# Kernel optimization log

Hardware: AMD Instinct MI355X
Metric: run time of the kernel (lower is better)

The kernel has to match this reference:

```python
import jax, jax.numpy as jnp
import numpy as np
from jax import lax

WINDOW_SIZE = 11
SIGMA = 1.5
MAX_VAL = 1.0


def _gaussian_kernel_2d(window_size: int, sigma: float) -> jnp.ndarray:
    coords = jnp.arange(window_size, dtype=jnp.float32) - window_size // 2
    g = jnp.exp(-coords ** 2 / (2.0 * sigma ** 2))
    g = g / g.sum()
    k2d = jnp.outer(g, g)
    return k2d / k2d.sum()  # [W, W]


def _depthwise_conv(x: jnp.ndarray, k2d: jnp.ndarray) -> jnp.ndarray:
    # x: [B, C, H, W]; depthwise (groups=C) conv with SAME padding
    C = x.shape[1]
    ws = k2d.shape[0]
    kernel = jnp.broadcast_to(k2d[None, None], (C, 1, ws, ws)).astype(x.dtype)  # [C,1,ws,ws]
    pad = ws // 2
    return lax.conv_general_dilated(
        x, kernel,
        window_strides=(1, 1),
        padding=((pad, pad), (pad, pad)),
        dimension_numbers=('NCHW', 'OIHW', 'NCHW'),
        feature_group_count=C,
    )


def setup_inputs() -> dict:
    key = jax.random.key(0)
    k1, k2 = jax.random.split(key)
    B, C, H, W = 16, 3, 512, 512
    sr = jax.random.uniform(k1, (B, C, H, W), dtype=jnp.float32)
    hr = jax.random.uniform(k2, (B, C, H, W), dtype=jnp.float32)
    return {"sr": sr, "hr": hr}


def reference(sr, hr):
    c1 = (0.01 * MAX_VAL) ** 2
    c2 = (0.03 * MAX_VAL) ** 2
    k2d = _gaussian_kernel_2d(WINDOW_SIZE, SIGMA)

    mu1 = _depthwise_conv(sr, k2d)
    mu2 = _depthwise_conv(hr, k2d)
    mu1_sq = mu1 ** 2
    mu2_sq = mu2 ** 2
    mu1_mu2 = mu1 * mu2
    sigma1_sq = _depthwise_conv(sr * sr, k2d) - mu1_sq
    sigma2_sq = _depthwise_conv(hr * hr, k2d) - mu2_sq
    sigma12 = _depthwise_conv(sr * hr, k2d) - mu1_mu2

    ssim_map = (2 * mu1_mu2 + c1) * (2 * sigma12 + c2) / (
        (mu1_sq + mu2_sq + c1) * (sigma1_sq + sigma2_sq + c2) + 1e-12)
    return 1.0 - ssim_map.mean()
```

## Files before the change

### kernel.cpp

```cpp
#include <hip/hip_runtime.h>


typedef __attribute__((ext_vector_type(2))) float  f32x2;
typedef __attribute__((ext_vector_type(4))) float  f32x4;
typedef __fp16 f16;
typedef __attribute__((ext_vector_type(2))) __fp16 h2v;
typedef __attribute__((ext_vector_type(4))) __fp16 h4;
typedef __attribute__((ext_vector_type(8))) __fp16 h8;

constexpr int IMG_H = 512;
constexpr int IMG_W = 512;
constexpr int PL    = IMG_H * IMG_W;
constexpr int NBC   = 48;
constexpr int TW    = 64;
constexpr int TH    = 32;
constexpr int NBLKX = IMG_W / TW;
constexpr int NBLKY = IMG_H / TH;
constexpr int NPERS = 1024;
constexpr int ITERS = NBLKX * NBLKY * NBC / NPERS;

constexpr int XP   = 104;
constexpr int XR   = 48;
constexpr int XQS  = XR * XP;
constexpr int HTP  = 72;
constexpr int HTQS = 64 * HTP;
constexpr int SMEMH = 4 * XQS;
static_assert(4 * HTQS <= SMEMH, "Ht must fit in X union");

constexpr float C1 = 1.0e-4f;
constexpr float C2 = 9.0e-4f;

__device__ const float GW[11] = {
    0.00102838f, 0.00759876f, 0.03600077f, 0.10936070f, 0.21300553f,
    0.26601172f, 0.21300553f, 0.10936070f, 0.03600077f, 0.00759876f,
    0.00102838f};

__device__ __forceinline__ h8 ldfrag(const f16* __restrict__ gtab, int base) {
    h8 b;
#pragma unroll
    for (int i = 0; i < 8; ++i) b[i] = gtab[base + i];
    return b;
}

__global__ __launch_bounds__(64) void ssim_init(double* acc) {
    if (threadIdx.x == 0) acc[0] = 0.0;
}

__global__ __launch_bounds__(256, 4) void ssim_main(const float* __restrict__ sr,
                                                    const float* __restrict__ hr,
                                                    double* __restrict__ sink,
                                                    int mode) {
    __shared__ __align__(16) f16 smem[SMEMH];
    __shared__ __align__(8)  f16 gtab[128];
    __shared__ float wsums[4];

    const int tid  = threadIdx.x;
    const int w    = tid >> 6;
    const int lane = tid & 63;
    const int l15  = lane & 15;
    const int grp8 = (lane >> 4) << 3;
    const int grp4 = (lane >> 4) << 2;

    const int bx  = blockIdx.x & 7;
    const int by  = (blockIdx.x >> 3) & 15;
    const int bc0 = blockIdx.x >> 7;
    const int gr0 = by * TH - 5;
    const int gc0 = bx * TW - 8;

    const float* __restrict__ srp = sr + (size_t)bc0 * PL;
    const float* __restrict__ hrp = hr + (size_t)bc0 * PL;
    const size_t PSTEP = (size_t)8 * PL;

    const int c8  = tid & 15;
    const int r0s = tid >> 4;
    unsigned okm = 0;
    int off[3];
#pragma unroll
    for (int t = 0; t < 3; ++t) {
        const int r  = r0s + 16 * t;
        const int gr = gr0 + r;
        const int gc = gc0 + c8 * 8;
        if ((c8 < 10) & (r < 42) &
            ((unsigned)gr < (unsigned)IMG_H) & ((unsigned)gc < (unsigned)IMG_W))
            okm |= (1u << t);
        off[t] = gr * IMG_W + gc;
    }

    if (tid < 128) {
        const int d = tid - 66;
        float v = 0.f;
        if ((unsigned)d <= 10u) v = GW[d];
        gtab[tid] = (f16)v;
    }

    float s16 = 0.f;
#pragma unroll
    for (int d = 0; d <= 10; ++d) s16 += (float)(f16)GW[d];
    const float rs = 1.0f / (s16 * s16);

    float4 La0[3], La1[3], Lb0[3], Lb1[3];
#pragma unroll
    for (int t = 0; t < 3; ++t) {
        La0[t] = La1[t] = Lb0[t] = Lb1[t] = (float4){0.f, 0.f, 0.f, 0.f};
        if (okm & (1u << t)) {
            const float4* pa = (const float4*)&srp[off[t]];
            const float4* pb = (const float4*)&hrp[off[t]];
            La0[t] = pa[0]; La1[t] = pa[1];
            Lb0[t] = pb[0]; Lb1[t] = pb[1];
        }
    }
    __syncthreads();

    const h8 bh = ldfrag(gtab, 63 + grp8 - l15);
    const h8 bv = ldfrag(gtab, 66 + grp8 - l15);

    float local = 0.f;

    for (int iter = 0; iter < ITERS; ++iter) {
        if (c8 < 10) {
#pragma unroll
            for (int t = 0; t < 3; ++t) {
                const int r = r0s + 16 * t;
                const f32x2* a0 = (const f32x2*)&La0[t];
                const f32x2* a1 = (const f32x2*)&La1[t];
                const f32x2* b0 = (const f32x2*)&Lb0[t];
                const f32x2* b1 = (const f32x2*)&Lb1[t];
                const f32x2 s0 = a0[0] * a0[0] + b0[0] * b0[0];
                const f32x2 s1 = a0[1] * a0[1] + b0[1] * b0[1];
                const f32x2 s2 = a1[0] * a1[0] + b1[0] * b1[0];
                const f32x2 s3 = a1[1] * a1[1] + b1[1] * b1[1];
                const f32x2 p0 = a0[0] * b0[0], p1 = a0[1] * b0[1];
                const f32x2 p2 = a1[0] * b1[0], p3 = a1[1] * b1[1];
                union { h2v h2[4]; h8 v; } uva, uvb, uss, uab;
                uva.h2[0] = __builtin_amdgcn_cvt_pkrtz(a0[0].x, a0[0].y);
                uva.h2[1] = __builtin_amdgcn_cvt_pkrtz(a0[1].x, a0[1].y);
                uva.h2[2] = __builtin_amdgcn_cvt_pkrtz(a1[0].x, a1[0].y);
                uva.h2[3] = __builtin_amdgcn_cvt_pkrtz(a1[1].x, a1[1].y);
                uvb.h2[0] = __builtin_amdgcn_cvt_pkrtz(b0[0].x, b0[0].y);
                uvb.h2[1] = __builtin_amdgcn_cvt_pkrtz(b0[1].x, b0[1].y);
                uvb.h2[2] = __builtin_amdgcn_cvt_pkrtz(b1[0].x, b1[0].y);
                uvb.h2[3] = __builtin_amdgcn_cvt_pkrtz(b1[1].x, b1[1].y);
                uss.h2[0] = __builtin_amdgcn_cvt_pkrtz(s0.x, s0.y);
                uss.h2[1] = __builtin_amdgcn_cvt_pkrtz(s1.x, s1.y);
                uss.h2[2] = __builtin_amdgcn_cvt_pkrtz(s2.x, s2.y);
                uss.h2[3] = __builtin_amdgcn_cvt_pkrtz(s3.x, s3.y);
                uab.h2[0] = __builtin_amdgcn_cvt_pkrtz(p0.x, p0.y);
                uab.h2[1] = __builtin_amdgcn_cvt_pkrtz(p1.x, p1.y);
                uab.h2[2] = __builtin_amdgcn_cvt_pkrtz(p2.x, p2.y);
                uab.h2[3] = __builtin_amdgcn_cvt_pkrtz(p3.x, p3.y);
                const int o = r * XP + c8 * 8;
                *(h8*)&smem[0 * XQS + o] = uva.v;
                *(h8*)&smem[1 * XQS + o] = uvb.v;
                *(h8*)&smem[2 * XQS + o] = uss.v;
                *(h8*)&smem[3 * XQS + o] = uab.v;
            }
        }
        __syncthreads();

        if (iter < ITERS - 1) {
            srp += PSTEP; hrp += PSTEP;
#pragma unroll
            for (int t = 0; t < 3; ++t) {
                if (okm & (1u << t)) {
                    const float4* pa = (const float4*)&srp[off[t]];
                    const float4* pb = (const float4*)&hrp[off[t]];
                    La0[t] = pa[0]; La1[t] = pa[1];
                    Lb0[t] = pb[0]; Lb1[t] = pb[1];
                }
            }
        }

        f32x4 acc[4][3] = {};
#pragma unroll
        for (int Mt = 0; Mt < 3; ++Mt) {
            const int arow = (16 * Mt + l15) * XP + 16 * w + grp8;
#pragma unroll
            for (int q = 0; q < 4; ++q) {
                const h8 af = *(const h8*)&smem[q * XQS + arow];
                acc[q][Mt] = __builtin_amdgcn_mfma_f32_16x16x32_f16(af, bh, acc[q][Mt], 0, 0, 0);
            }
        }
        __syncthreads();

#pragma unroll
        for (int q = 0; q < 4; ++q) {
#pragma unroll
            for (int Mt = 0; Mt < 3; ++Mt) {
                union { h2v h2[2]; h4 v; } u;
                u.h2[0] = __builtin_amdgcn_cvt_pkrtz(acc[q][Mt][0], acc[q][Mt][1]);
                u.h2[1] = __builtin_amdgcn_cvt_pkrtz(acc[q][Mt][2], acc[q][Mt][3]);
                *(h4*)&smem[q * HTQS + (16 * w + l15) * HTP + 16 * Mt + grp4] = u.v;
            }
        }

        f32x4 acc2[4][2] = {};
        const int abase = (16 * w + l15) * HTP + grp8;
#pragma unroll
        for (int q = 0; q < 4; ++q) {
            const h8 a0 = *(const h8*)&smem[q * HTQS + abase];
            const h8 a1 = *(const h8*)&smem[q * HTQS + abase + 16];
            acc2[q][0] = __builtin_amdgcn_mfma_f32_16x16x32_f16(a0, bv, acc2[q][0], 0, 0, 0);
            acc2[q][1] = __builtin_amdgcn_mfma_f32_16x16x32_f16(a1, bv, acc2[q][1], 0, 0, 0);
        }

#pragma unroll
        for (int nt = 0; nt < 2; ++nt) {
            const f32x4 m1 = acc2[0][nt] * rs;
            const f32x4 m2 = acc2[1][nt] * rs;
            const f32x4 S  = acc2[2][nt] * rs;
            const f32x4 pp = acc2[3][nt] * rs;
            const f32x4 mu1s = m1 * m1, mu2s = m2 * m2, mu12 = m1 * m2;
            const f32x4 sg12 = pp - mu12;
            const f32x4 sgs  = S - mu1s - mu2s;
            const f32x4 num = (2.f * mu12 + C1) * (2.f * sg12 + C2);
            const f32x4 den = (mu1s + mu2s + C1) * (sgs + C2) + 1e-12f;
#pragma unroll
            for (int e = 0; e < 4; ++e)
                local += num[e] * __builtin_amdgcn_rcpf(den[e]);
        }
        __syncthreads();
    }

#pragma unroll
    for (int offr = 32; offr > 0; offr >>= 1)
        local += __shfl_down(local, offr, 64);
    if ((tid & 63) == 0) wsums[tid >> 6] = local;
    __syncthreads();
    if (tid == 0) {
        const double bsum = (double)(wsums[0] + wsums[1] + wsums[2] + wsums[3]);
        if (mode == 0) {
            sink[blockIdx.x] = bsum;
        } else {
            atomicAdd(sink, bsum);
        }
    }
}

__global__ __launch_bounds__(256) void ssim_finalize(const double* __restrict__ partial,
                                                     float* __restrict__ out, int count) {
    __shared__ double ws[4];
    double s = 0.0;
    for (int i = threadIdx.x; i < count; i += 256) s += partial[i];
#pragma unroll
    for (int off = 32; off > 0; off >>= 1)
        s += __shfl_down(s, off, 64);
    const int lane = threadIdx.x & 63, wave = threadIdx.x >> 6;
    if (lane == 0) ws[wave] = s;
    __syncthreads();
    if (threadIdx.x == 0) {
        const double tot = ws[0] + ws[1] + ws[2] + ws[3];
        const double n = (double)NBC * IMG_H * IMG_W;
        out[0] = (float)(1.0 - tot / n);
    }
}

extern "C" void kernel_launch(void* const* d_in, const int* in_sizes, int n_in,
                              void* d_out, int out_size, void* d_ws, size_t ws_size,
                              hipStream_t stream) {
    const float* sr = (const float*)d_in[0];
    const float* hr = (const float*)d_in[1];
    float* out = (float*)d_out;

    if (ws_size >= (size_t)NPERS * sizeof(double)) {
        double* partial = (double*)d_ws;
        ssim_main<<<dim3(NPERS), dim3(256), 0, stream>>>(sr, hr, partial, 0);
        ssim_finalize<<<dim3(1), dim3(256), 0, stream>>>(partial, out, NPERS);
    } else {
        double* acc = (double*)d_ws;
        ssim_init<<<dim3(1), dim3(64), 0, stream>>>(acc);
        ssim_main<<<dim3(NPERS), dim3(256), 0, stream>>>(sr, hr, acc, 1);
        ssim_finalize<<<dim3(1), dim3(256), 0, stream>>>(acc, out, 1);
    }
}
```

Before: 130.0 us.

## Load MFMA A-fragments directly from global, drop input LDS staging and barriers

Each lane now loads its horizontal-pass MFMA A fragment straight from global memory into registers, converts it to fp16 and feeds the MFMA. This removes the shared-memory staging of the four input planes and all block-level barriers, since each wave only touches its own LDS rows for the transposed intermediate. Shared memory shrinks, occupancy is raised to 5 blocks per CU, and the persistent grid becomes 1280 blocks striding over planes by 10. The cost is that overlapping halo columns are loaded redundantly by several waves, and the software prefetch of the next plane is lost.

```diff
diff --git a/kernel.cpp b/kernel.cpp
--- a/kernel.cpp
+++ b/kernel.cpp
@@ -14,18 +14,11 @@
 constexpr int NBC   = 48;
 constexpr int TW    = 64;
 constexpr int TH    = 32;
-constexpr int NBLKX = IMG_W / TW;
-constexpr int NBLKY = IMG_H / TH;
-constexpr int NPERS = 1024;
-constexpr int ITERS = NBLKX * NBLKY * NBC / NPERS;
-
-constexpr int XP   = 104;
-constexpr int XR   = 48;
-constexpr int XQS  = XR * XP;
-constexpr int HTP  = 72;
-constexpr int HTQS = 64 * HTP;
-constexpr int SMEMH = 4 * XQS;
-static_assert(4 * HTQS <= SMEMH, "Ht must fit in X union");
+constexpr int NPERS = 1280;
+
+constexpr int HTP   = 56;
+constexpr int HTQS  = 64 * HTP;
+constexpr int SMEMH = 4 * HTQS;
 
 constexpr float C1 = 1.0e-4f;
 constexpr float C2 = 9.0e-4f;
@@ -46,7 +39,7 @@
     if (threadIdx.x == 0) acc[0] = 0.0;
 }
 
-__global__ __launch_bounds__(256, 4) void ssim_main(const float* __restrict__ sr,
+__global__ __launch_bounds__(256, 5) void ssim_main(const float* __restrict__ sr,
                                                     const float* __restrict__ hr,
                                                     double* __restrict__ sink,
                                                     int mode) {
@@ -67,24 +60,9 @@
     const int gr0 = by * TH - 5;
     const int gc0 = bx * TW - 8;
 
-    const float* __restrict__ srp = sr + (size_t)bc0 * PL;
-    const float* __restrict__ hrp = hr + (size_t)bc0 * PL;
-    const size_t PSTEP = (size_t)8 * PL;
-
-    const int c8  = tid & 15;
-    const int r0s = tid >> 4;
-    unsigned okm = 0;
-    int off[3];
-#pragma unroll
-    for (int t = 0; t < 3; ++t) {
-        const int r  = r0s + 16 * t;
-        const int gr = gr0 + r;
-        const int gc = gc0 + c8 * 8;
-        if ((c8 < 10) & (r < 42) &
-            ((unsigned)gr < (unsigned)IMG_H) & ((unsigned)gc < (unsigned)IMG_W))
-            okm |= (1u << t);
-        off[t] = gr * IMG_W + gc;
-    }
+    const int colh = gc0 + 16 * w + grp8;
+    const bool cok = (unsigned)colh < (unsigned)IMG_W;
+    const int rb   = gr0 + l15;
 
     if (tid < 128) {
         const int d = tid - 66;
@@ -98,17 +76,6 @@
     for (int d = 0; d <= 10; ++d) s16 += (float)(f16)GW[d];
     const float rs = 1.0f / (s16 * s16);
 
-    float4 La0[3], La1[3], Lb0[3], Lb1[3];
-#pragma unroll
-    for (int t = 0; t < 3; ++t) {
-        La0[t] = La1[t] = Lb0[t] = Lb1[t] = (float4){0.f, 0.f, 0.f, 0.f};
-        if (okm & (1u << t)) {
-            const float4* pa = (const float4*)&srp[off[t]];
-            const float4* pb = (const float4*)&hrp[off[t]];
-            La0[t] = pa[0]; La1[t] = pa[1];
-            Lb0[t] = pb[0]; Lb1[t] = pb[1];
-        }
-    }
     __syncthreads();
 
     const h8 bh = ldfrag(gtab, 63 + grp8 - l15);
@@ -116,72 +83,58 @@
 
     float local = 0.f;
 
-    for (int iter = 0; iter < ITERS; ++iter) {
-        if (c8 < 10) {
-#pragma unroll
-            for (int t = 0; t < 3; ++t) {
-                const int r = r0s + 16 * t;
-                const f32x2* a0 = (const f32x2*)&La0[t];
-                const f32x2* a1 = (const f32x2*)&La1[t];
-                const f32x2* b0 = (const f32x2*)&Lb0[t];
-                const f32x2* b1 = (const f32x2*)&Lb1[t];
-                const f32x2 s0 = a0[0] * a0[0] + b0[0] * b0[0];
-                const f32x2 s1 = a0[1] * a0[1] + b0[1] * b0[1];
-                const f32x2 s2 = a1[0] * a1[0] + b1[0] * b1[0];
-                const f32x2 s3 = a1[1] * a1[1] + b1[1] * b1[1];
-                const f32x2 p0 = a0[0] * b0[0], p1 = a0[1] * b0[1];
-                const f32x2 p2 = a1[0] * b1[0], p3 = a1[1] * b1[1];
-                union { h2v h2[4]; h8 v; } uva, uvb, uss, uab;
-                uva.h2[0] = __builtin_amdgcn_cvt_pkrtz(a0[0].x, a0[0].y);
-                uva.h2[1] = __builtin_amdgcn_cvt_pkrtz(a0[1].x, a0[1].y);
-                uva.h2[2] = __builtin_amdgcn_cvt_pkrtz(a1[0].x, a1[0].y);
-                uva.h2[3] = __builtin_amdgcn_cvt_pkrtz(a1[1].x, a1[1].y);
-                uvb.h2[0] = __builtin_amdgcn_cvt_pkrtz(b0[0].x, b0[0].y);
-                uvb.h2[1] = __builtin_amdgcn_cvt_pkrtz(b0[1].x, b0[1].y);
-                uvb.h2[2] = __builtin_amdgcn_cvt_pkrtz(b1[0].x, b1[0].y);
-                uvb.h2[3] = __builtin_amdgcn_cvt_pkrtz(b1[1].x, b1[1].y);
-                uss.h2[0] = __builtin_amdgcn_cvt_pkrtz(s0.x, s0.y);
-                uss.h2[1] = __builtin_amdgcn_cvt_pkrtz(s1.x, s1.y);
-                uss.h2[2] = __builtin_amdgcn_cvt_pkrtz(s2.x, s2.y);
-                uss.h2[3] = __builtin_amdgcn_cvt_pkrtz(s3.x, s3.y);
-                uab.h2[0] = __builtin_amdgcn_cvt_pkrtz(p0.x, p0.y);
-                uab.h2[1] = __builtin_amdgcn_cvt_pkrtz(p1.x, p1.y);
-                uab.h2[2] = __builtin_amdgcn_cvt_pkrtz(p2.x, p2.y);
-                uab.h2[3] = __builtin_amdgcn_cvt_pkrtz(p3.x, p3.y);
-                const int o = r * XP + c8 * 8;
-                *(h8*)&smem[0 * XQS + o] = uva.v;
-                *(h8*)&smem[1 * XQS + o] = uvb.v;
-                *(h8*)&smem[2 * XQS + o] = uss.v;
-                *(h8*)&smem[3 * XQS + o] = uab.v;
+    for (int bc = bc0; bc < NBC; bc += 10) {
+        const float* __restrict__ srp = sr + (size_t)bc * PL;
+        const float* __restrict__ hrp = hr + (size_t)bc * PL;
+
+        f32x4 acc[4][3] = {};
+#pragma unroll
+        for (int Mt = 0; Mt < 3; ++Mt) {
+            const int r  = rb + 16 * Mt;
+            const bool ok = cok & ((unsigned)r < (unsigned)IMG_H);
+            float4 a0, a1, b0, b1;
+            a0 = a1 = b0 = b1 = (float4){0.f, 0.f, 0.f, 0.f};
+            if (ok) {
+                const float4* pa = (const float4*)&srp[r * IMG_W + colh];
+                const float4* pb = (const float4*)&hrp[r * IMG_W + colh];
+                a0 = pa[0]; a1 = pa[1];
+                b0 = pb[0]; b1 = pb[1];
             }
-        }
-        __syncthreads();
-
-        if (iter < ITERS - 1) {
-            srp += PSTEP; hrp += PSTEP;
-#pragma unroll
-            for (int t = 0; t < 3; ++t) {
-                if (okm & (1u << t)) {
-                    const float4* pa = (const float4*)&srp[off[t]];
-                    const float4* pb = (const float4*)&hrp[off[t]];
-                    La0[t] = pa[0]; La1[t] = pa[1];
-                    Lb0[t] = pb[0]; Lb1[t] = pb[1];
-                }
-            }
-        }
-
-        f32x4 acc[4][3] = {};
-#pragma unroll
-        for (int Mt = 0; Mt < 3; ++Mt) {
-            const int arow = (16 * Mt + l15) * XP + 16 * w + grp8;
-#pragma unroll
-            for (int q = 0; q < 4; ++q) {
-                const h8 af = *(const h8*)&smem[q * XQS + arow];
-                acc[q][Mt] = __builtin_amdgcn_mfma_f32_16x16x32_f16(af, bh, acc[q][Mt], 0, 0, 0);
-            }
-        }
-        __syncthreads();
-
+            const f32x2* A0 = (const f32x2*)&a0;
+            const f32x2* A1 = (const f32x2*)&a1;
+            const f32x2* B0 = (const f32x2*)&b0;
+            const f32x2* B1 = (const f32x2*)&b1;
+            const f32x2 s0 = A0[0] * A0[0] + B0[0] * B0[0];
+            const f32x2 s1 = A0[1] * A0[1] + B0[1] * B0[1];
+            const f32x2 s2 = A1[0] * A1[0] + B1[0] * B1[0];
+            const f32x2 s3 = A1[1] * A1[1] + B1[1] * B1[1];
+            const f32x2 p0 = A0[0] * B0[0], p1 = A0[1] * B0[1];
+            const f32x2 p2 = A1[0] * B1[0], p3 = A1[1] * B1[1];
+            union { h2v h2[4]; h8 v; } fa, fb, fs, fp;
+            fa.h2[0] = __builtin_amdgcn_cvt_pkrtz(A0[0].x, A0[0].y);
+            fa.h2[1] = __builtin_amdgcn_cvt_pkrtz(A0[1].x, A0[1].y);
+            fa.h2[2] = __builtin_amdgcn_cvt_pkrtz(A1[0].x, A1[0].y);
+            fa.h2[3] = __builtin_amdgcn_cvt_pkrtz(A1[1].x, A1[1].y);
+            fb.h2[0] = __builtin_amdgcn_cvt_pkrtz(B0[0].x, B0[0].y);
+            fb.h2[1] = __builtin_amdgcn_cvt_pkrtz(B0[1].x, B0[1].y);
+            fb.h2[2] = __builtin_amdgcn_cvt_pkrtz(B1[0].x, B1[0].y);
+            fb.h2[3] = __builtin_amdgcn_cvt_pkrtz(B1[1].x, B1[1].y);
+            fs.h2[0] = __builtin_amdgcn_cvt_pkrtz(s0.x, s0.y);
+            fs.h2[1] = __builtin_amdgcn_cvt_pkrtz(s1.x, s1.y);
+            fs.h2[2] = __builtin_amdgcn_cvt_pkrtz(s2.x, s2.y);
+            fs.h2[3] = __builtin_amdgcn_cvt_pkrtz(s3.x, s3.y);
+            fp.h2[0] = __builtin_amdgcn_cvt_pkrtz(p0.x, p0.y);
+            fp.h2[1] = __builtin_amdgcn_cvt_pkrtz(p1.x, p1.y);
+            fp.h2[2] = __builtin_amdgcn_cvt_pkrtz(p2.x, p2.y);
+            fp.h2[3] = __builtin_amdgcn_cvt_pkrtz(p3.x, p3.y);
+            acc[0][Mt] = __builtin_amdgcn_mfma_f32_16x16x32_f16(fa.v, bh, acc[0][Mt], 0, 0, 0);
+            acc[1][Mt] = __builtin_amdgcn_mfma_f32_16x16x32_f16(fb.v, bh, acc[1][Mt], 0, 0, 0);
+            acc[2][Mt] = __builtin_amdgcn_mfma_f32_16x16x32_f16(fs.v, bh, acc[2][Mt], 0, 0, 0);
+            acc[3][Mt] = __builtin_amdgcn_mfma_f32_16x16x32_f16(fp.v, bh, acc[3][Mt], 0, 0, 0);
+        }
+
+        f32x4 acc2[4][2];
+        const int cbase = (16 * w + l15) * HTP;
 #pragma unroll
         for (int q = 0; q < 4; ++q) {
 #pragma unroll
@@ -189,18 +142,13 @@
                 union { h2v h2[2]; h4 v; } u;
                 u.h2[0] = __builtin_amdgcn_cvt_pkrtz(acc[q][Mt][0], acc[q][Mt][1]);
                 u.h2[1] = __builtin_amdgcn_cvt_pkrtz(acc[q][Mt][2], acc[q][Mt][3]);
-                *(h4*)&smem[q * HTQS + (16 * w + l15) * HTP + 16 * Mt + grp4] = u.v;
+                *(h4*)&smem[q * HTQS + cbase + 16 * Mt + grp4] = u.v;
             }
-        }
-
-        f32x4 acc2[4][2] = {};
-        const int abase = (16 * w + l15) * HTP + grp8;
-#pragma unroll
-        for (int q = 0; q < 4; ++q) {
-            const h8 a0 = *(const h8*)&smem[q * HTQS + abase];
-            const h8 a1 = *(const h8*)&smem[q * HTQS + abase + 16];
-            acc2[q][0] = __builtin_amdgcn_mfma_f32_16x16x32_f16(a0, bv, acc2[q][0], 0, 0, 0);
-            acc2[q][1] = __builtin_amdgcn_mfma_f32_16x16x32_f16(a1, bv, acc2[q][1], 0, 0, 0);
+            const h8 a0 = *(const h8*)&smem[q * HTQS + cbase + grp8];
+            const h8 a1 = *(const h8*)&smem[q * HTQS + cbase + grp8 + 16];
+            const f32x4 z = {0.f, 0.f, 0.f, 0.f};
+            acc2[q][0] = __builtin_amdgcn_mfma_f32_16x16x32_f16(a0, bv, z, 0, 0, 0);
+            acc2[q][1] = __builtin_amdgcn_mfma_f32_16x16x32_f16(a1, bv, z, 0, 0, 0);
         }
 
 #pragma unroll
@@ -218,7 +166,6 @@
             for (int e = 0; e < 4; ++e)
                 local += num[e] * __builtin_amdgcn_rcpf(den[e]);
         }
-        __syncthreads();
     }
 
 #pragma unroll
```

Result: slower. 141.7 us (+9.0%).
